# Performance work log

Measured on AMD Instinct MI355X. Metric: run time of the kernel, lower is better.

The kernel has to match this reference:

```python
import jax, jax.numpy as jnp
import numpy as np
import math

N_HEAD = 16
N_FEAT = 1024
O_FEAT = 1024
D_K = N_FEAT // N_HEAD


def setup_inputs() -> dict:
    key = jax.random.key(0)
    ks = jax.random.split(key, 11)
    B, L, DIN = 4, 2048, 1024
    s_in = 1.0 / math.sqrt(DIN)
    s_f = 1.0 / math.sqrt(N_FEAT)
    return {
        "query": jax.random.normal(ks[0], (B, L, DIN), jnp.float32),
        "key": jax.random.normal(ks[1], (B, L, DIN), jnp.float32),
        "value": jax.random.normal(ks[2], (B, L, DIN), jnp.float32),
        "Wq": jax.random.uniform(ks[3], (DIN, N_FEAT), jnp.float32, -s_in, s_in),
        "bq": jax.random.uniform(ks[4], (N_FEAT,), jnp.float32, -s_in, s_in),
        "Wk": jax.random.uniform(ks[5], (DIN, N_FEAT), jnp.float32, -s_in, s_in),
        "bk": jax.random.uniform(ks[6], (N_FEAT,), jnp.float32, -s_in, s_in),
        "Wv": jax.random.uniform(ks[7], (DIN, N_FEAT), jnp.float32, -s_in, s_in),
        "bv": jax.random.uniform(ks[8], (N_FEAT,), jnp.float32, -s_in, s_in),
        "Wo": jax.random.uniform(ks[9], (N_FEAT, O_FEAT), jnp.float32, -s_f, s_f),
        "bo": jax.random.uniform(ks[10], (O_FEAT,), jnp.float32, -s_f, s_f),
    }


def reference(query, key, value, Wq, bq, Wk, bk, Wv, bv, Wo, bo):
    B = query.shape[0]
    # QKV projections -> [B, H, L, Dk]
    def proj(x, W, b):
        y = x @ W + b
        return y.reshape(B, -1, N_HEAD, D_K).transpose(0, 2, 1, 3)
    q = proj(query, Wq, bq)
    k = proj(key, Wk, bk)
    v = proj(value, Wv, bv)
    # naive attention: full [B,H,Lq,Lk] scores
    scores = jnp.einsum("bhqd,bhkd->bhqk", q, k) / math.sqrt(D_K)
    attn = jax.nn.softmax(scores, axis=-1)  # dropout_rate=0 -> identity
    x = jnp.einsum("bhqk,bhkd->bhqd", attn, v)
    x = x.transpose(0, 2, 1, 3).reshape(B, -1, N_FEAT)
    return x @ Wo + bo
```

## Files before the change

kernel.cpp:

```cpp
#include <hip/hip_runtime.h>
#include <hip/hip_bf16.h>

#define DM 1024
#define LQ 2048

typedef __attribute__((ext_vector_type(8))) short short8;
typedef __attribute__((ext_vector_type(4))) float floatx4;

#define MFMA16(a, b, c) __builtin_amdgcn_mfma_f32_16x16x32_bf16((a), (b), (c), 0, 0, 0)
#define BAR() __builtin_amdgcn_s_barrier()
#define FENCE() asm volatile("" ::: "memory")
#define VWAIT4() asm volatile("s_waitcnt vmcnt(4)" ::: "memory")
#define VWAIT0() asm volatile("s_waitcnt vmcnt(0)" ::: "memory")

__device__ __forceinline__ unsigned short f2b(float f) {
  union { float f; unsigned u; } x; x.f = f;
  unsigned u = x.u;
  unsigned r = (u + 0x7fffu + ((u >> 16) & 1u)) >> 16;
  return (unsigned short)r;
}

__device__ __forceinline__ unsigned cvt_pk(float lo, float hi) {
  unsigned r;
  asm("v_cvt_pk_bf16_f32 %0, %1, %2" : "=v"(r) : "v"(lo), "v"(hi));
  return r;
}
__device__ __forceinline__ uint4 pack16(float4 a, float4 b) {
  return make_uint4(cvt_pk(a.x, a.y), cvt_pk(a.z, a.w),
                    cvt_pk(b.x, b.y), cvt_pk(b.z, b.w));
}

__device__ __forceinline__ void gl_lds16(const void* g, void* l) {
  __builtin_amdgcn_global_load_lds(
      (const __attribute__((address_space(1))) void*)g,
      (__attribute__((address_space(3))) void*)l, 16, 0, 0);
}

__device__ __forceinline__ void xcd_tiles(int bx, int by, int* m0, int* n0) {
  int flat = bx + (by << 3);
  int xcd = flat & 7;
  int loc = flat >> 3;
  *m0 = (xcd * 8 + (loc >> 3)) * 128;
  *n0 = (loc & 7) * 128;
}

__global__ __launch_bounds__(256) void cvt3(
    const float* __restrict__ A0, const float* __restrict__ A1,
    const float* __restrict__ A2,
    unsigned short* __restrict__ O0, unsigned short* __restrict__ O1,
    unsigned short* __restrict__ O2) {
  const float* s = (blockIdx.z == 0) ? A0 : (blockIdx.z == 1) ? A1 : A2;
  unsigned short* d = (blockIdx.z == 0) ? O0 : (blockIdx.z == 1) ? O1 : O2;
  size_t i = ((size_t)blockIdx.x * 256 + threadIdx.x) * 8;
  float4 f0 = *(const float4*)(s + i);
  float4 f1 = *(const float4*)(s + i + 4);
  *(uint4*)(d + i) = pack16(f0, f1);
}

__global__ __launch_bounds__(256) void transpose_w4(
    const float* __restrict__ W0, const float* __restrict__ W1,
    const float* __restrict__ W2, const float* __restrict__ W3,
    unsigned short* __restrict__ T0, unsigned short* __restrict__ T1,
    unsigned short* __restrict__ T2, unsigned short* __restrict__ T3) {
  __shared__ unsigned short t[64][65];
  const float* src; unsigned short* dst;
  switch (blockIdx.z) {
    case 0: src = W0; dst = T0; break;
    case 1: src = W1; dst = T1; break;
    case 2: src = W2; dst = T2; break;
    default: src = W3; dst = T3; break;
  }
  const int x = threadIdx.x & 63;
  const int y4 = threadIdx.x >> 6;
  const int c0 = blockIdx.x * 64;
  const int r0 = blockIdx.y * 64;
#pragma unroll
  for (int i = 0; i < 16; ++i) {
    int r = y4 * 16 + i;
    t[r][x] = f2b(src[(size_t)(r0 + r) * 1024 + c0 + x]);
  }
  __syncthreads();
#pragma unroll
  for (int i = 0; i < 16; ++i) {
    int r = y4 * 16 + i;
    dst[(size_t)(c0 + r) * 1024 + r0 + x] = t[x][r];
  }
}


__global__ __launch_bounds__(256) void gemm_qkv(
    const unsigned short* __restrict__ Aq, const unsigned short* __restrict__ Ak,
    const unsigned short* __restrict__ Av,
    const unsigned short* __restrict__ BtQ, const unsigned short* __restrict__ BtK,
    const unsigned short* __restrict__ BtV,
    const float* __restrict__ bq, const float* __restrict__ bk,
    const float* __restrict__ bv,
    unsigned short* __restrict__ Qb, unsigned short* __restrict__ Kb,
    unsigned short* __restrict__ Vt) {
  const int K = 1024, N = 1024;
  __shared__ unsigned short As[2][128 * 32];
  __shared__ unsigned short Bs[2][128 * 32];
  const int z = blockIdx.z;
  const unsigned short* A; const unsigned short* Bt; const float* bias;
  if (z == 0) { A = Aq; Bt = BtQ; bias = bq; }
  else if (z == 1) { A = Ak; Bt = BtK; bias = bk; }
  else { A = Av; Bt = BtV; bias = bv; }

  const int tid = threadIdx.x;
  const int wave = tid >> 6;
  const int lane = tid & 63;
  const int fm = lane & 15;
  const int quad = lane >> 4;
  int m0, n0;
  xcd_tiles(blockIdx.x, blockIdx.y, &m0, &n0);
  const int wm = (wave >> 1) * 64;
  const int wn = (wave & 1) * 64;

  floatx4 acc[4][4];
#pragma unroll
  for (int i = 0; i < 4; ++i)
#pragma unroll
    for (int j = 0; j < 4; ++j) acc[i][j] = (floatx4){0.f, 0.f, 0.f, 0.f};

  const int srow = lane >> 2;
  const int scol = (lane & 3) * 8;
  const unsigned short* Ag = A + (size_t)(m0 + wave * 32 + srow) * K + scol;
  const unsigned short* Bg = Bt + (size_t)(n0 + wave * 32 + srow) * K + scol;
  const int stA = wave * 32 * 32;

#pragma unroll
  for (int t = 0; t < 2; ++t) {
    gl_lds16(Ag + t * 32, &As[t][stA]);
    gl_lds16(Ag + t * 32 + (size_t)16 * K, &As[t][stA + 16 * 32]);
    gl_lds16(Bg + t * 32, &Bs[t][stA]);
    gl_lds16(Bg + t * 32 + (size_t)16 * K, &Bs[t][stA + 16 * 32]);
  }

#pragma unroll 1
  for (int t = 0; t < 30; ++t) {
    const int buf = t & 1;
    VWAIT4();
    BAR();
    FENCE();
    short8 a[4], b[4];
#pragma unroll
    for (int i = 0; i < 4; ++i)
      a[i] = *(const short8*)&As[buf][(wm + i * 16 + fm) * 32 + quad * 8];
#pragma unroll
    for (int j = 0; j < 4; ++j)
      b[j] = *(const short8*)&Bs[buf][(wn + j * 16 + fm) * 32 + quad * 8];
#pragma unroll
    for (int i = 0; i < 4; ++i)
#pragma unroll
      for (int j = 0; j < 4; ++j) acc[i][j] = MFMA16(a[i], b[j], acc[i][j]);
    BAR();
    FENCE();
    const int tn = t + 2;
    gl_lds16(Ag + tn * 32, &As[buf][stA]);
    gl_lds16(Ag + tn * 32 + (size_t)16 * K, &As[buf][stA + 16 * 32]);
    gl_lds16(Bg + tn * 32, &Bs[buf][stA]);
    gl_lds16(Bg + tn * 32 + (size_t)16 * K, &Bs[buf][stA + 16 * 32]);
  }
#pragma unroll
  for (int t = 30; t < 32; ++t) {
    if (t == 30) VWAIT4(); else VWAIT0();
    BAR();
    FENCE();
    const int buf = t & 1;
    short8 a[4], b[4];
#pragma unroll
    for (int i = 0; i < 4; ++i)
      a[i] = *(const short8*)&As[buf][(wm + i * 16 + fm) * 32 + quad * 8];
#pragma unroll
    for (int j = 0; j < 4; ++j)
      b[j] = *(const short8*)&Bs[buf][(wn + j * 16 + fm) * 32 + quad * 8];
#pragma unroll
    for (int i = 0; i < 4; ++i)
#pragma unroll
      for (int j = 0; j < 4; ++j) acc[i][j] = MFMA16(a[i], b[j], acc[i][j]);
  }

  float bvv[4];
#pragma unroll
  for (int j = 0; j < 4; ++j) bvv[j] = bias[n0 + wn + j * 16 + fm];

  if (z < 2) {
    const float sc = (z == 0) ? 0.1803368801111204f : 1.0f;
    unsigned short* C = (z == 0) ? Qb : Kb;
#pragma unroll
    for (int i = 0; i < 4; ++i) {
      int row = m0 + wm + i * 16 + quad * 4;
#pragma unroll
      for (int j = 0; j < 4; ++j) {
        int col = n0 + wn + j * 16 + fm;
#pragma unroll
        for (int r = 0; r < 4; ++r)
          C[(size_t)(row + r) * N + col] = f2b((acc[i][j][r] + bvv[j]) * sc);
      }
    }
  } else {
#pragma unroll
    for (int i = 0; i < 4; ++i) {
      int row = m0 + wm + i * 16 + quad * 4;
      int b = row >> 11, l = row & 2047;
#pragma unroll
      for (int j = 0; j < 4; ++j) {
        int col = n0 + wn + j * 16 + fm;
        int h = col >> 6, d = col & 63;
        uint2 pk;
        pk.x = cvt_pk(acc[i][j][0] + bvv[j], acc[i][j][1] + bvv[j]);
        pk.y = cvt_pk(acc[i][j][2] + bvv[j], acc[i][j][3] + bvv[j]);
        *(uint2*)&Vt[(((size_t)b * 16 + h) * 64 + d) * 2048 + l] = pk;
      }
    }
  }
}

__global__ __launch_bounds__(256) void gemm_bt_bias_f32(
    const unsigned short* __restrict__ A, const unsigned short* __restrict__ Bt,
    const float* __restrict__ bias, float* __restrict__ C,
    int M, int N, int K) {
  __shared__ unsigned short As[2][128 * 32];
  __shared__ unsigned short Bs[2][128 * 32];
  const int tid = threadIdx.x;
  const int wave = tid >> 6;
  const int lane = tid & 63;
  const int fm = lane & 15;
  const int quad = lane >> 4;
  int m0, n0;
  xcd_tiles(blockIdx.x, blockIdx.y, &m0, &n0);
  const int wm = (wave >> 1) * 64;
  const int wn = (wave & 1) * 64;

  floatx4 acc[4][4];
#pragma unroll
  for (int i = 0; i < 4; ++i)
#pragma unroll
    for (int j = 0; j < 4; ++j) acc[i][j] = (floatx4){0.f, 0.f, 0.f, 0.f};

  const int srow = lane >> 2;
  const int scol = (lane & 3) * 8;
  const unsigned short* Ag = A + (size_t)(m0 + wave * 32 + srow) * K + scol;
  const unsigned short* Bg = Bt + (size_t)(n0 + wave * 32 + srow) * K + scol;
  const int stA = wave * 32 * 32;

#pragma unroll
  for (int t = 0; t < 2; ++t) {
    gl_lds16(Ag + t * 32, &As[t][stA]);
    gl_lds16(Ag + t * 32 + (size_t)16 * K, &As[t][stA + 16 * 32]);
    gl_lds16(Bg + t * 32, &Bs[t][stA]);
    gl_lds16(Bg + t * 32 + (size_t)16 * K, &Bs[t][stA + 16 * 32]);
  }

#pragma unroll 1
  for (int t = 0; t < 30; ++t) {
    const int buf = t & 1;
    VWAIT4();
    BAR();
    FENCE();
    short8 a[4], b[4];
#pragma unroll
    for (int i = 0; i < 4; ++i)
      a[i] = *(const short8*)&As[buf][(wm + i * 16 + fm) * 32 + quad * 8];
#pragma unroll
    for (int j = 0; j < 4; ++j)
      b[j] = *(const short8*)&Bs[buf][(wn + j * 16 + fm) * 32 + quad * 8];
#pragma unroll
    for (int i = 0; i < 4; ++i)
#pragma unroll
      for (int j = 0; j < 4; ++j) acc[i][j] = MFMA16(a[i], b[j], acc[i][j]);
    BAR();
    FENCE();
    const int tn = t + 2;
    gl_lds16(Ag + tn * 32, &As[buf][stA]);
    gl_lds16(Ag + tn * 32 + (size_t)16 * K, &As[buf][stA + 16 * 32]);
    gl_lds16(Bg + tn * 32, &Bs[buf][stA]);
    gl_lds16(Bg + tn * 32 + (size_t)16 * K, &Bs[buf][stA + 16 * 32]);
  }
#pragma unroll
  for (int t = 30; t < 32; ++t) {
    if (t == 30) VWAIT4(); else VWAIT0();
    BAR();
    FENCE();
    const int buf = t & 1;
    short8 a[4], b[4];
#pragma unroll
    for (int i = 0; i < 4; ++i)
      a[i] = *(const short8*)&As[buf][(wm + i * 16 + fm) * 32 + quad * 8];
#pragma unroll
    for (int j = 0; j < 4; ++j)
      b[j] = *(const short8*)&Bs[buf][(wn + j * 16 + fm) * 32 + quad * 8];
#pragma unroll
    for (int i = 0; i < 4; ++i)
#pragma unroll
      for (int j = 0; j < 4; ++j) acc[i][j] = MFMA16(a[i], b[j], acc[i][j]);
  }

  float bv[4];
#pragma unroll
  for (int j = 0; j < 4; ++j) bv[j] = bias[n0 + wn + j * 16 + fm];
#pragma unroll
  for (int i = 0; i < 4; ++i) {
    int row = m0 + wm + i * 16 + quad * 4;
#pragma unroll
    for (int j = 0; j < 4; ++j) {
      int col = n0 + wn + j * 16 + fm;
#pragma unroll
      for (int r = 0; r < 4; ++r)
        C[(size_t)(row + r) * N + col] = acc[i][j][r] + bv[j];
    }
  }
}

__global__ __launch_bounds__(256, 4) void attn_kernel(
    const unsigned short* Qb, const unsigned short* __restrict__ Kb,
    const unsigned short* __restrict__ Vtg, unsigned short* Xb) {
  __shared__ unsigned short Ks[64 * 72];
  __shared__ unsigned short Vts[64 * 72];
  __shared__ unsigned short Ps[4 * 32 * 72];
  unsigned short* Qs = Ps;

  const int tid = threadIdx.x;
  const int wave = tid >> 6;
  const int lane = tid & 63;
  const int fm = lane & 15;
  const int quad = lane >> 4;
  const int flat = blockIdx.x + (blockIdx.y << 4);
  const int loc = flat >> 3;
  const int qt = loc & 15;
  const int bh = ((flat & 7) << 3) | (loc >> 4);
  const size_t base = (size_t)(bh >> 4) * (LQ * DM) + (size_t)(bh & 15) * 64;
  const unsigned short* Vg = Vtg + (size_t)bh * 64 * 2048;
  const int q0 = qt * 128;

#pragma unroll
  for (int it = 0; it < 4; ++it) {
    int idx = it * 256 + tid;
    int r = idx >> 3;
    int cc = (idx & 7) * 8;
    *(short8*)&Qs[r * 72 + cc] =
        *(const short8*)(Qb + base + (size_t)(q0 + r) * DM + cc);
  }
  __syncthreads();
  short8 qf[2][2];
#pragma unroll
  for (int mt = 0; mt < 2; ++mt)
#pragma unroll
    for (int ks = 0; ks < 2; ++ks)
      qf[mt][ks] = *(const short8*)&Qs[(wave * 32 + mt * 16 + fm) * 72 + ks * 32 + quad * 8];
  __syncthreads();

  short8 ones;
#pragma unroll
  for (int i = 0; i < 8; ++i) ones[i] = (short)0x3F80;

  floatx4 lacc[2];
  lacc[0] = (floatx4){0.f, 0.f, 0.f, 0.f};
  lacc[1] = (floatx4){0.f, 0.f, 0.f, 0.f};
  floatx4 oacc[4][2];
#pragma unroll
  for (int dt = 0; dt < 4; ++dt)
#pragma unroll
    for (int mt = 0; mt < 2; ++mt) oacc[dt][mt] = (floatx4){0.f, 0.f, 0.f, 0.f};

  unsigned short* Pw = &Ps[wave * 32 * 72];

  const int srow0 = tid >> 3;
  const int scc = (tid & 7) * 8;
  short8 kr[2], vr[2];
#pragma unroll
  for (int it = 0; it < 2; ++it) {
    int row = it * 32 + srow0;
    kr[it] = *(const short8*)(Kb + base + (size_t)row * DM + scc);
    vr[it] = *(const short8*)(Vg + (size_t)row * 2048 + scc);
  }

  for (int kt = 0; kt < 32; ++kt) {
    __syncthreads();
#pragma unroll
    for (int it = 0; it < 2; ++it) {
      int row = it * 32 + srow0;
      *(short8*)&Ks[row * 72 + scc] = kr[it];
      *(short8*)&Vts[row * 72 + scc] = vr[it];
    }
    __syncthreads();
    if (kt < 31) {
      int k0n = (kt + 1) * 64;
#pragma unroll
      for (int it = 0; it < 2; ++it) {
        int row = it * 32 + srow0;
        kr[it] = *(const short8*)(Kb + base + (size_t)(k0n + row) * DM + scc);
        vr[it] = *(const short8*)(Vg + (size_t)row * 2048 + k0n + scc);
      }
    }

    floatx4 sacc[4][2];
#pragma unroll
    for (int jt = 0; jt < 4; ++jt)
#pragma unroll
      for (int mt = 0; mt < 2; ++mt) sacc[jt][mt] = (floatx4){0.f, 0.f, 0.f, 0.f};
    __builtin_amdgcn_s_setprio(1);
#pragma unroll
    for (int jt = 0; jt < 4; ++jt) {
      short8 k0f = *(const short8*)&Ks[(jt * 16 + fm) * 72 + quad * 8];
      short8 k1f = *(const short8*)&Ks[(jt * 16 + fm) * 72 + 32 + quad * 8];
#pragma unroll
      for (int mt = 0; mt < 2; ++mt) {
        sacc[jt][mt] = MFMA16(k0f, qf[mt][0], sacc[jt][mt]);
        sacc[jt][mt] = MFMA16(k1f, qf[mt][1], sacc[jt][mt]);
      }
    }
    __builtin_amdgcn_s_setprio(0);

#pragma unroll
    for (int mt = 0; mt < 2; ++mt) {
      int rowoff = (mt * 16 + fm) * 72;
#pragma unroll
      for (int jt = 0; jt < 4; ++jt) {
        float p0 = __builtin_amdgcn_exp2f(sacc[jt][mt][0]);
        float p1 = __builtin_amdgcn_exp2f(sacc[jt][mt][1]);
        float p2 = __builtin_amdgcn_exp2f(sacc[jt][mt][2]);
        float p3 = __builtin_amdgcn_exp2f(sacc[jt][mt][3]);
        uint2 pk;
        pk.x = cvt_pk(p0, p1);
        pk.y = cvt_pk(p2, p3);
        *(uint2*)&Pw[rowoff + jt * 16 + quad * 4] = pk;
      }
    }

    __threadfence_block();

    __builtin_amdgcn_s_setprio(1);
#pragma unroll
    for (int ks = 0; ks < 2; ++ks) {
      short8 pf0 = *(const short8*)&Pw[fm * 72 + ks * 32 + quad * 8];
      short8 pf1 = *(const short8*)&Pw[(16 + fm) * 72 + ks * 32 + quad * 8];
      lacc[0] = MFMA16(ones, pf0, lacc[0]);
      lacc[1] = MFMA16(ones, pf1, lacc[1]);
#pragma unroll
      for (int dt = 0; dt < 4; ++dt) {
        short8 vf = *(const short8*)&Vts[(dt * 16 + fm) * 72 + ks * 32 + quad * 8];
        oacc[dt][0] = MFMA16(vf, pf0, oacc[dt][0]);
        oacc[dt][1] = MFMA16(vf, pf1, oacc[dt][1]);
      }
    }
    __builtin_amdgcn_s_setprio(0);
  }

  float inv[2];
  inv[0] = 1.0f / lacc[0][0];
  inv[1] = 1.0f / lacc[1][0];

#pragma unroll
  for (int mt = 0; mt < 2; ++mt) {
    int q = q0 + wave * 32 + mt * 16 + fm;
#pragma unroll
    for (int dt = 0; dt < 4; ++dt) {
      uint2 o;
      o.x = cvt_pk(oacc[dt][mt][0] * inv[mt], oacc[dt][mt][1] * inv[mt]);
      o.y = cvt_pk(oacc[dt][mt][2] * inv[mt], oacc[dt][mt][3] * inv[mt]);
      *(uint2*)&Xb[base + (size_t)q * DM + dt * 16 + quad * 4] = o;
    }
  }
}

extern "C" void kernel_launch(void* const* d_in, const int* in_sizes, int n_in,
                              void* d_out, int out_size, void* d_ws, size_t ws_size,
                              hipStream_t stream) {
  const float* q_in = (const float*)d_in[0];
  const float* k_in = (const float*)d_in[1];
  const float* v_in = (const float*)d_in[2];
  const float* Wq = (const float*)d_in[3];
  const float* bq = (const float*)d_in[4];
  const float* Wk = (const float*)d_in[5];
  const float* bk = (const float*)d_in[6];
  const float* Wv = (const float*)d_in[7];
  const float* bv = (const float*)d_in[8];
  const float* Wo = (const float*)d_in[9];
  const float* bo = (const float*)d_in[10];
  float* out = (float*)d_out;

  char* w = (char*)d_ws;
  unsigned short* WqT = (unsigned short*)w; w += 1024 * 1024 * 2;
  unsigned short* WkT = (unsigned short*)w; w += 1024 * 1024 * 2;
  unsigned short* WvT = (unsigned short*)w; w += 1024 * 1024 * 2;
  unsigned short* WoT = (unsigned short*)w; w += 1024 * 1024 * 2;
  unsigned short* Qb  = (unsigned short*)w; w += (size_t)8192 * 1024 * 2;
  unsigned short* Kb  = (unsigned short*)w; w += (size_t)8192 * 1024 * 2;
  unsigned short* Vt  = (unsigned short*)w; w += (size_t)8192 * 1024 * 2;
  unsigned short* Qa  = (unsigned short*)w; w += (size_t)8192 * 1024 * 2;
  unsigned short* Ka  = (unsigned short*)w; w += (size_t)8192 * 1024 * 2;
  unsigned short* Va  = (unsigned short*)w; w += (size_t)8192 * 1024 * 2;
  unsigned short* Xb  = Qb;

  transpose_w4<<<dim3(16, 16, 4), 256, 0, stream>>>(Wq, Wk, Wv, Wo,
                                                    WqT, WkT, WvT, WoT);

  cvt3<<<dim3(4096, 1, 3), 256, 0, stream>>>(q_in, k_in, v_in, Qa, Ka, Va);

  gemm_qkv<<<dim3(8, 64, 3), 256, 0, stream>>>(
      Qa, Ka, Va, WqT, WkT, WvT, bq, bk, bv, Qb, Kb, Vt);

  attn_kernel<<<dim3(16, 64), 256, 0, stream>>>(Qb, Kb, Vt, Xb);

  gemm_bt_bias_f32<<<dim3(8, 64), 256, 0, stream>>>(Xb, WoT, bo, out, 8192, 1024, 1024);
}
```

Baseline: 347.5 us.

## Pass softmax P fragments via permlane swaps instead of LDS round-trip

The exponentiated score tile is now rearranged into the PV MFMA operand layout with v_permlane32/16_swap in registers, instead of being written to and re-read from a per-wave LDS buffer. This removes the P buffer, so shared memory shrinks to one array holding Q (at startup), then K and V, and launch bounds rise to 6 blocks per CU for higher occupancy. The costs are extra permlane instructions and a correctness dependence on the lane-swap mapping matching the MFMA fragment layout. The higher occupancy target may also squeeze registers.

```diff
diff --git a/kernel.cpp b/kernel.cpp
--- a/kernel.cpp
+++ b/kernel.cpp
@@ -312,13 +312,10 @@
   }
 }
 
-__global__ __launch_bounds__(256, 4) void attn_kernel(
+__global__ __launch_bounds__(256, 6) void attn_kernel(
     const unsigned short* Qb, const unsigned short* __restrict__ Kb,
     const unsigned short* __restrict__ Vtg, unsigned short* Xb) {
-  __shared__ unsigned short Ks[64 * 72];
-  __shared__ unsigned short Vts[64 * 72];
-  __shared__ unsigned short Ps[4 * 32 * 72];
-  unsigned short* Qs = Ps;
+  __shared__ unsigned short lds[9216];
 
   const int tid = threadIdx.x;
   const int wave = tid >> 6;
@@ -338,7 +335,7 @@
     int idx = it * 256 + tid;
     int r = idx >> 3;
     int cc = (idx & 7) * 8;
-    *(short8*)&Qs[r * 72 + cc] =
+    *(short8*)&lds[r * 72 + cc] =
         *(const short8*)(Qb + base + (size_t)(q0 + r) * DM + cc);
   }
   __syncthreads();
@@ -347,7 +344,7 @@
   for (int mt = 0; mt < 2; ++mt)
 #pragma unroll
     for (int ks = 0; ks < 2; ++ks)
-      qf[mt][ks] = *(const short8*)&Qs[(wave * 32 + mt * 16 + fm) * 72 + ks * 32 + quad * 8];
+      qf[mt][ks] = *(const short8*)&lds[(wave * 32 + mt * 16 + fm) * 72 + ks * 32 + quad * 8];
   __syncthreads();
 
   short8 ones;
@@ -363,8 +360,6 @@
 #pragma unroll
     for (int mt = 0; mt < 2; ++mt) oacc[dt][mt] = (floatx4){0.f, 0.f, 0.f, 0.f};
 
-  unsigned short* Pw = &Ps[wave * 32 * 72];
-
   const int srow0 = tid >> 3;
   const int scc = (tid & 7) * 8;
   short8 kr[2], vr[2];
@@ -380,8 +375,8 @@
 #pragma unroll
     for (int it = 0; it < 2; ++it) {
       int row = it * 32 + srow0;
-      *(short8*)&Ks[row * 72 + scc] = kr[it];
-      *(short8*)&Vts[row * 72 + scc] = vr[it];
+      *(short8*)&lds[row * 72 + scc] = kr[it];
+      *(short8*)&lds[4608 + row * 72 + scc] = vr[it];
     }
     __syncthreads();
     if (kt < 31) {
@@ -402,8 +397,8 @@
     __builtin_amdgcn_s_setprio(1);
 #pragma unroll
     for (int jt = 0; jt < 4; ++jt) {
-      short8 k0f = *(const short8*)&Ks[(jt * 16 + fm) * 72 + quad * 8];
-      short8 k1f = *(const short8*)&Ks[(jt * 16 + fm) * 72 + 32 + quad * 8];
+      short8 k0f = *(const short8*)&lds[(jt * 16 + fm) * 72 + quad * 8];
+      short8 k1f = *(const short8*)&lds[(jt * 16 + fm) * 72 + 32 + quad * 8];
 #pragma unroll
       for (int mt = 0; mt < 2; ++mt) {
         sacc[jt][mt] = MFMA16(k0f, qf[mt][0], sacc[jt][mt]);
@@ -412,34 +407,53 @@
     }
     __builtin_amdgcn_s_setprio(0);
 
+    unsigned pfd[2][2][4];
 #pragma unroll
     for (int mt = 0; mt < 2; ++mt) {
-      int rowoff = (mt * 16 + fm) * 72;
+      unsigned c0[4], c1[4];
 #pragma unroll
       for (int jt = 0; jt < 4; ++jt) {
         float p0 = __builtin_amdgcn_exp2f(sacc[jt][mt][0]);
         float p1 = __builtin_amdgcn_exp2f(sacc[jt][mt][1]);
         float p2 = __builtin_amdgcn_exp2f(sacc[jt][mt][2]);
         float p3 = __builtin_amdgcn_exp2f(sacc[jt][mt][3]);
-        uint2 pk;
-        pk.x = cvt_pk(p0, p1);
-        pk.y = cvt_pk(p2, p3);
-        *(uint2*)&Pw[rowoff + jt * 16 + quad * 4] = pk;
-      }
-    }
-
-    __threadfence_block();
+        c0[jt] = cvt_pk(p0, p1);
+        c1[jt] = cvt_pk(p2, p3);
+      }
+#pragma unroll
+      for (int ks = 0; ks < 2; ++ks) {
+        unsigned a0 = c0[2 * ks], b0 = c0[2 * ks + 1];
+        unsigned a1 = c1[2 * ks], b1 = c1[2 * ks + 1];
+        asm("v_permlane32_swap_b32 %0, %1" : "+v"(a0), "+v"(b0));
+        asm("v_permlane16_swap_b32 %0, %1" : "+v"(a0), "+v"(b0));
+        asm("v_permlane32_swap_b32 %0, %1" : "+v"(a1), "+v"(b1));
+        asm("v_permlane16_swap_b32 %0, %1" : "+v"(a1), "+v"(b1));
+        pfd[ks][mt][0] = a0;
+        pfd[ks][mt][1] = a1;
+        pfd[ks][mt][2] = b0;
+        pfd[ks][mt][3] = b1;
+      }
+    }
 
     __builtin_amdgcn_s_setprio(1);
 #pragma unroll
     for (int ks = 0; ks < 2; ++ks) {
-      short8 pf0 = *(const short8*)&Pw[fm * 72 + ks * 32 + quad * 8];
-      short8 pf1 = *(const short8*)&Pw[(16 + fm) * 72 + ks * 32 + quad * 8];
+      short8 pf0, pf1;
+      {
+        union { uint4 u; short8 s; } t;
+        t.u = make_uint4(pfd[ks][0][0], pfd[ks][0][1], pfd[ks][0][2], pfd[ks][0][3]);
+        pf0 = t.s;
+      }
+      {
+        union { uint4 u; short8 s; } t;
+        t.u = make_uint4(pfd[ks][1][0], pfd[ks][1][1], pfd[ks][1][2], pfd[ks][1][3]);
+        pf1 = t.s;
+      }
       lacc[0] = MFMA16(ones, pf0, lacc[0]);
       lacc[1] = MFMA16(ones, pf1, lacc[1]);
 #pragma unroll
       for (int dt = 0; dt < 4; ++dt) {
-        short8 vf = *(const short8*)&Vts[(dt * 16 + fm) * 72 + ks * 32 + quad * 8];
+        short8 vf = *(const short8*)&lds[4608 + (dt * 16 + fm) * 72 + ks * 32 + quad * 8];
         oacc[dt][0] = MFMA16(vf, pf0, oacc[dt][0]);
         oacc[dt][1] = MFMA16(vf, pf1, oacc[dt][1]);
       }
```

Result: slower. 739.9 us (+113.0%).
